# Kernel optimization log

Hardware: AMD Instinct MI355X
Metric: run time of the kernel (lower is better)

## Reference

```python
import jax, jax.numpy as jnp
import numpy as np

H_OUT = 512
W_OUT = 512


def _leaky(x):
    return jnp.where(x >= 0, x, 0.2 * x)


def _spline(cp, out_size):
    # cp: [B, R, N] control points -> [B, R, out_size] cubic Hermite interp
    N = cp.shape[-1]
    nseg = N - 1
    eps = 1e-3
    t = jnp.linspace(eps, 1.0 - eps, out_size)
    ts = t * nseg
    seg = jnp.clip(jnp.floor(ts).astype(jnp.int32), 0, nseg - 1)
    tau = jnp.clip(ts - seg.astype(ts.dtype), 0.0, 0.9999)
    t2 = tau * tau
    t3 = t2 * tau
    h00 = 2 * t3 - 3 * t2 + 1
    h10 = t3 - 2 * t2 + tau
    h01 = -2 * t3 + 3 * t2
    h11 = t3 - t2
    # central-difference tangents, scaled by 1/num_segments
    m = jnp.concatenate([
        (cp[..., 1:2] - cp[..., 0:1]) * 0.5,
        (cp[..., 2:] - cp[..., :-2]) * 0.5,
        (cp[..., -1:] - cp[..., -2:-1]) * 0.5,
    ], axis=-1) / nseg
    seg1 = jnp.clip(seg + 1, 0, N - 1)
    pk = cp[..., seg]
    pk1 = cp[..., seg1]
    mk = m[..., seg]
    mk1 = m[..., seg1]
    return h00 * pk + h10 * mk + h01 * pk1 + h11 * mk1


def _gen(feats, w1, b1, w2, b2):
    # batched per-rank 2-layer MLP: feats [B,R,D], w1 [R,D,Hd], w2 [R,Hd,C]
    hdn = _leaky(jnp.einsum('brd,rdh->brh', feats, w1) + b1[None])
    return jnp.einsum('brh,rhc->brc', hdn, w2) + b2[None]


def setup_inputs() -> dict:
    key = jax.random.key(0)
    ks = iter(jax.random.split(key, 40))
    def rn(shape, s=0.05):
        return jax.random.normal(next(ks), shape, jnp.float32) * s
    B, D, Hd = 64, 768, 256
    Rm, Ra, CX, CY = 16, 8, 24, 24
    Rt = Rm + Ra
    inp = {
        'h': jax.random.normal(next(ks), (B, D), jnp.float32),
        'rank_emb': rn((Rt, Hd), 0.1),
        'st_w1': rn((D, 2 * Hd)), 'st_b1': jnp.zeros((2 * Hd,), jnp.float32),
        'st_w2': rn((2 * Hd, Hd)), 'st_b2': jnp.zeros((Hd,), jnp.float32),
        'rm_w1': rn((Rt, 2 * Hd, Hd)), 'rm_b1': jnp.zeros((Rt, Hd), jnp.float32),
        'rm_w2': rn((Rt, Hd, Hd)), 'rm_b2': jnp.zeros((Rt, Hd), jnp.float32),
        'mx_w1': rn((Rm, Hd, Hd)), 'mx_b1': jnp.zeros((Rm, Hd), jnp.float32),
        'mx_w2': rn((Rm, Hd, CX)), 'mx_b2': jnp.zeros((Rm, CX), jnp.float32),
        'my_w1': rn((Rm, Hd, Hd)), 'my_b1': jnp.zeros((Rm, Hd), jnp.float32),
        'my_w2': rn((Rm, Hd, CY)), 'my_b2': jnp.zeros((Rm, CY), jnp.float32),
        'ax_w1': rn((Ra, Hd, Hd)), 'ax_b1': jnp.zeros((Ra, Hd), jnp.float32),
        'ax_w2': rn((Ra, Hd, CX)), 'ax_b2': jnp.zeros((Ra, CX), jnp.float32),
        'ay_w1': rn((Ra, Hd, Hd)), 'ay_b1': jnp.zeros((Ra, Hd), jnp.float32),
        'ay_w2': rn((Ra, Hd, CY)), 'ay_b2': jnp.zeros((Ra, CY), jnp.float32),
        'mult_w': jnp.ones((Rm,), jnp.float32) / Rm,
        'addx_w': jnp.ones((Ra,), jnp.float32) / Ra * 0.5,
        'addy_w': jnp.ones((Ra,), jnp.float32) / Ra * 0.5,
        'gbias': jnp.asarray(0.5, jnp.float32),
    }
    return inp


def reference(h, rank_emb, st_w1, st_b1, st_w2, st_b2,
              rm_w1, rm_b1, rm_w2, rm_b2,
              mx_w1, mx_b1, mx_w2, mx_b2,
              my_w1, my_b1, my_w2, my_b2,
              ax_w1, ax_b1, ax_w2, ax_b2,
              ay_w1, ay_b1, ay_w2, ay_b2,
              mult_w, addx_w, addy_w, gbias):
    B = h.shape[0]
    Rt = rank_emb.shape[0]
    Rm = mx_w1.shape[0]
    # shared conditioning
    shared = _leaky(h @ st_w1 + st_b1) @ st_w2 + st_b2  # [B, Hd]
    comb = jnp.concatenate([
        jnp.broadcast_to(shared[:, None, :], (B, Rt, shared.shape[-1])),
        jnp.broadcast_to(rank_emb[None], (B, Rt, rank_emb.shape[-1])),
    ], axis=-1)  # [B, Rt, 2*Hd]
    rf = _gen(comb, rm_w1, rm_b1, rm_w2, rm_b2)  # [B, Rt, Hd]
    fm, fa = rf[:, :Rm], rf[:, Rm:]
    Px_m = _gen(fm, mx_w1, mx_b1, mx_w2, mx_b2)  # [B, Rm, CX]
    Py_m = _gen(fm, my_w1, my_b1, my_w2, my_b2)
    Px_a = _gen(fa, ax_w1, ax_b1, ax_w2, ax_b2)
    Py_a = _gen(fa, ay_w1, ay_b1, ay_w2, ay_b2)
    u = _spline(Px_m, W_OUT)   # [B, Rm, W]
    v = _spline(Py_m, H_OUT)   # [B, Rm, H]
    a_x = _spline(Px_a, W_OUT)
    b_y = _spline(Py_a, H_OUT)
    depth_mult = jnp.einsum('brw,brh,r->bhw', u, v, jax.nn.softmax(mult_w))
    dx = jnp.einsum('brw,r->bw', a_x, jax.nn.softmax(addx_w))
    dy = jnp.einsum('brh,r->bh', b_y, jax.nn.softmax(addy_w))
    depth = depth_mult + dx[:, None, :] + dy[:, :, None] + gbias
    return depth[:, None]  # [B, 1, H, W]
```

## Files before the change

kernel.cpp:

```cpp
#include <hip/hip_runtime.h>


__device__ __forceinline__ float leaky(float v) { return v >= 0.f ? v : 0.2f * v; }

__global__ __launch_bounds__(256, 2) void l1_kernel(
    const float* __restrict__ h, const float* __restrict__ W,
    const float* __restrict__ bias, float* __restrict__ outp)
{
    __shared__ __align__(16) float a_lds[128][34];
    __shared__ __align__(16) float w_lds[128][34];
    const int tid = threadIdx.x;
    const int x = blockIdx.x, z = blockIdx.z;
    const int b0 = (x & 1) * 32, n0 = (x >> 1) * 32;
    const int nq = tid & 15, bq = tid >> 4;
    const int k0 = z * 128;
    float a00, a01, a10, a11;
    if (z == 0) {
        float bv0 = bias[n0 + nq * 2], bv1 = bias[n0 + nq * 2 + 1];
        a00 = bv0; a01 = bv1; a10 = bv0; a11 = bv1;
    } else { a00 = a01 = a10 = a11 = 0.f; }
    #pragma unroll
    for (int j = 0; j < 16; ++j) {
        int idx = tid + j * 256;
        int k = idx & 127, c = idx >> 7;
        a_lds[k][c] = h[(size_t)(b0 + c) * 768 + k0 + k];
        int n = idx & 31, kk = idx >> 5;
        w_lds[kk][n] = W[(size_t)(k0 + kk) * 512 + n0 + n];
    }
    __syncthreads();
    #pragma unroll 32
    for (int kk = 0; kk < 128; ++kk) {
        float2 a = *(const float2*)&a_lds[kk][bq * 2];
        float2 w = *(const float2*)&w_lds[kk][nq * 2];
        a00 += a.x * w.x; a01 += a.x * w.y;
        a10 += a.y * w.x; a11 += a.y * w.y;
    }
    float* ob = outp + (size_t)z * 32768;
    ob[(size_t)(b0 + bq * 2) * 512 + n0 + nq * 2]         = a00;
    ob[(size_t)(b0 + bq * 2) * 512 + n0 + nq * 2 + 1]     = a01;
    ob[(size_t)(b0 + bq * 2 + 1) * 512 + n0 + nq * 2]     = a10;
    ob[(size_t)(b0 + bq * 2 + 1) * 512 + n0 + nq * 2 + 1] = a11;
}

__global__ __launch_bounds__(512, 1) void mega_kernel(
    const float* __restrict__ hid1p,
    const float* __restrict__ st_w2, const float* __restrict__ st_b2,
    const float* __restrict__ rank_emb,
    const float* __restrict__ rm_w1, const float* __restrict__ rm_b1,
    const float* __restrict__ rm_w2, const float* __restrict__ rm_b2,
    const float* __restrict__ mx_w1, const float* __restrict__ mx_b1,
    const float* __restrict__ mx_w2, const float* __restrict__ mx_b2,
    const float* __restrict__ my_w1, const float* __restrict__ my_b1,
    const float* __restrict__ my_w2, const float* __restrict__ my_b2,
    const float* __restrict__ ax_w1, const float* __restrict__ ax_b1,
    const float* __restrict__ ax_w2, const float* __restrict__ ax_b2,
    const float* __restrict__ ay_w1, const float* __restrict__ ay_b1,
    const float* __restrict__ ay_w2, const float* __restrict__ ay_b2,
    float* __restrict__ Pcat)
{
    __shared__ __align__(16) float hid_s[8][512];
    __shared__ __align__(16) float sh_s[8][256];
    __shared__ __align__(16) float hdn_s[8][256];
    __shared__ __align__(16) float rf_s[8][256];
    __shared__ __align__(16) float hc_s[2][8][256];
    __shared__ float re_s[256];
    __shared__ float remb_s[256];
    const int tid = threadIdx.x;
    const int blk = blockIdx.x;
    const int r = blk % 24;
    const int bt = blk / 24;
    const int b0 = bt * 8;
    const int col = tid & 255, rh = tid >> 8;
    const int r0 = rh * 4;

    {
        const float4* hp = (const float4*)hid1p;
        #pragma unroll
        for (int i = 0; i < 2; ++i) {
            int idx = tid + i * 512;
            int row = idx >> 7, j4 = idx & 127;
            size_t off = (size_t)(b0 + row) * 128 + j4;
            float4 v0 = hp[off],            v1 = hp[8192 + off],  v2 = hp[16384 + off];
            float4 v3 = hp[24576 + off],    v4 = hp[32768 + off], v5 = hp[40960 + off];
            float4 s;
            s.x = leaky(v0.x + v1.x + v2.x + v3.x + v4.x + v5.x);
            s.y = leaky(v0.y + v1.y + v2.y + v3.y + v4.y + v5.y);
            s.z = leaky(v0.z + v1.z + v2.z + v3.z + v4.z + v5.z);
            s.w = leaky(v0.w + v1.w + v2.w + v3.w + v4.w + v5.w);
            ((float4*)&hid_s[row][0])[j4] = s;
        }
    }
    if (tid < 256) remb_s[tid] = rank_emb[r * 256 + tid];
    __syncthreads();

    {
        float bv = st_b2[col];
        float a0 = bv, a1 = bv, a2 = bv, a3 = bv;
        const float* wp = st_w2 + col;
        #pragma unroll 4
        for (int d = 0; d < 512; d += 4) {
            float w0 = wp[(size_t)(d + 0) * 256], w1 = wp[(size_t)(d + 1) * 256];
            float w2 = wp[(size_t)(d + 2) * 256], w3 = wp[(size_t)(d + 3) * 256];
            float4 s0 = *(const float4*)&hid_s[r0 + 0][d];
            float4 s1 = *(const float4*)&hid_s[r0 + 1][d];
            float4 s2 = *(const float4*)&hid_s[r0 + 2][d];
            float4 s3 = *(const float4*)&hid_s[r0 + 3][d];
            a0 += s0.x * w0 + s0.y * w1 + s0.z * w2 + s0.w * w3;
            a1 += s1.x * w0 + s1.y * w1 + s1.z * w2 + s1.w * w3;
            a2 += s2.x * w0 + s2.y * w1 + s2.z * w2 + s2.w * w3;
            a3 += s3.x * w0 + s3.y * w1 + s3.z * w2 + s3.w * w3;
        }
        sh_s[r0 + 0][col] = a0; sh_s[r0 + 1][col] = a1;
        sh_s[r0 + 2][col] = a2; sh_s[r0 + 3][col] = a3;
    }
    __syncthreads();

    if (tid < 256) {
        float rb = rm_b1[r * 256 + col];
        const float* wb = rm_w1 + ((size_t)r * 512 + 256) * 256 + col;
        #pragma unroll 4
        for (int d = 0; d < 256; d += 4) {
            float w0 = wb[(size_t)(d + 0) * 256], w1 = wb[(size_t)(d + 1) * 256];
            float w2 = wb[(size_t)(d + 2) * 256], w3 = wb[(size_t)(d + 3) * 256];
            float4 e = *(const float4*)&remb_s[d];
            rb += e.x * w0 + e.y * w1 + e.z * w2 + e.w * w3;
        }
        re_s[col] = rb;
    }
    __syncthreads();

    {
        float bv = re_s[col];
        float a0 = bv, a1 = bv, a2 = bv, a3 = bv;
        const float* wp = rm_w1 + (size_t)r * 512 * 256 + col;
        #pragma unroll 4
        for (int d = 0; d < 256; d += 4) {
            float w0 = wp[(size_t)(d + 0) * 256], w1 = wp[(size_t)(d + 1) * 256];
            float w2 = wp[(size_t)(d + 2) * 256], w3 = wp[(size_t)(d + 3) * 256];
            float4 s0 = *(const float4*)&sh_s[r0 + 0][d];
            float4 s1 = *(const float4*)&sh_s[r0 + 1][d];
            float4 s2 = *(const float4*)&sh_s[r0 + 2][d];
            float4 s3 = *(const float4*)&sh_s[r0 + 3][d];
            a0 += s0.x * w0 + s0.y * w1 + s0.z * w2 + s0.w * w3;
            a1 += s1.x * w0 + s1.y * w1 + s1.z * w2 + s1.w * w3;
            a2 += s2.x * w0 + s2.y * w1 + s2.z * w2 + s2.w * w3;
            a3 += s3.x * w0 + s3.y * w1 + s3.z * w2 + s3.w * w3;
        }
        hdn_s[r0 + 0][col] = leaky(a0); hdn_s[r0 + 1][col] = leaky(a1);
        hdn_s[r0 + 2][col] = leaky(a2); hdn_s[r0 + 3][col] = leaky(a3);
    }
    __syncthreads();

    {
        float bv = rm_b2[r * 256 + col];
        float a0 = bv, a1 = bv, a2 = bv, a3 = bv;
        const float* wp = rm_w2 + (size_t)r * 65536 + col;
        #pragma unroll 4
        for (int d = 0; d < 256; d += 4) {
            float w0 = wp[(size_t)(d + 0) * 256], w1 = wp[(size_t)(d + 1) * 256];
            float w2 = wp[(size_t)(d + 2) * 256], w3 = wp[(size_t)(d + 3) * 256];
            float4 s0 = *(const float4*)&hdn_s[r0 + 0][d];
            float4 s1 = *(const float4*)&hdn_s[r0 + 1][d];
            float4 s2 = *(const float4*)&hdn_s[r0 + 2][d];
            float4 s3 = *(const float4*)&hdn_s[r0 + 3][d];
            a0 += s0.x * w0 + s0.y * w1 + s0.z * w2 + s0.w * w3;
            a1 += s1.x * w0 + s1.y * w1 + s1.z * w2 + s1.w * w3;
            a2 += s2.x * w0 + s2.y * w1 + s2.z * w2 + s2.w * w3;
            a3 += s3.x * w0 + s3.y * w1 + s3.z * w2 + s3.w * w3;
        }
        rf_s[r0 + 0][col] = a0; rf_s[r0 + 1][col] = a1;
        rf_s[r0 + 2][col] = a2; rf_s[r0 + 3][col] = a3;
    }
    __syncthreads();

    const float *W1, *B1, *W2, *B2; int y;
    if (r < 16) {
        if (rh == 0) { y = r;      W1 = mx_w1 + (size_t)r * 65536;  B1 = mx_b1 + r * 256;  W2 = mx_w2 + (size_t)r * 6144;  B2 = mx_b2 + r * 24; }
        else         { y = 16 + r; W1 = my_w1 + (size_t)r * 65536;  B1 = my_b1 + r * 256;  W2 = my_w2 + (size_t)r * 6144;  B2 = my_b2 + r * 24; }
    } else {
        int rw = r - 16;
        if (rh == 0) { y = 32 + rw; W1 = ax_w1 + (size_t)rw * 65536; B1 = ax_b1 + rw * 256; W2 = ax_w2 + (size_t)rw * 6144; B2 = ax_b2 + rw * 24; }
        else         { y = 40 + rw; W1 = ay_w1 + (size_t)rw * 65536; B1 = ay_b1 + rw * 256; W2 = ay_w2 + (size_t)rw * 6144; B2 = ay_b2 + rw * 24; }
    }

    {
        float bv = B1[col];
        float acc[8];
        #pragma unroll
        for (int i = 0; i < 8; ++i) acc[i] = bv;
        const float* wp = W1 + col;
        #pragma unroll 2
        for (int d = 0; d < 256; d += 4) {
            float w0 = wp[(size_t)(d + 0) * 256], w1 = wp[(size_t)(d + 1) * 256];
            float w2 = wp[(size_t)(d + 2) * 256], w3 = wp[(size_t)(d + 3) * 256];
            #pragma unroll
            for (int i = 0; i < 8; ++i) {
                float4 s = *(const float4*)&rf_s[i][d];
                acc[i] += s.x * w0 + s.y * w1 + s.z * w2 + s.w * w3;
            }
        }
        #pragma unroll
        for (int i = 0; i < 8; ++i) hc_s[rh][i][col] = leaky(acc[i]);
    }
    __syncthreads();

    if (col < 192) {
        int row = col / 24, cj = col - row * 24;
        float acc = B2[cj];
        const float* wp = W2 + cj;
        #pragma unroll 4
        for (int d = 0; d < 256; d += 4) {
            float w0 = wp[(size_t)(d + 0) * 24], w1 = wp[(size_t)(d + 1) * 24];
            float w2 = wp[(size_t)(d + 2) * 24], w3 = wp[(size_t)(d + 3) * 24];
            float4 s = *(const float4*)&hc_s[rh][row][d];
            acc += s.x * w0 + s.y * w1 + s.z * w2 + s.w * w3;
        }
        Pcat[(size_t)(b0 + row) * 1152 + y * 24 + cj] = acc;
    }
}

__global__ __launch_bounds__(256, 2) void depth_fused_kernel(
    const float* __restrict__ Pcat,
    const float* __restrict__ mult_w, const float* __restrict__ addx_w,
    const float* __restrict__ addy_w, const float* __restrict__ gbias,
    float* __restrict__ out)
{
    __shared__ float cp[48][25];
    __shared__ float sw[33];
    __shared__ __align__(16) float u_s[16][132];
    __shared__ __align__(16) float v_s[16][132];
    __shared__ float dx_s[128], dy_s[128];
    const int tid = threadIdx.x;
    const int b = blockIdx.z, h0 = blockIdx.y * 128, w0 = blockIdx.x * 128;
    for (int idx = tid; idx < 1152; idx += 256)
        cp[idx / 24][idx % 24] = Pcat[(size_t)b * 1152 + idx];
    if (tid == 0) {
        float e[16], m, s;
        m = -1e30f; for (int i = 0; i < 16; ++i) m = fmaxf(m, mult_w[i]);
        s = 0.f;    for (int i = 0; i < 16; ++i) { e[i] = __expf(mult_w[i] - m); s += e[i]; }
        for (int i = 0; i < 16; ++i) sw[i] = e[i] / s;
        m = -1e30f; for (int i = 0; i < 8; ++i) m = fmaxf(m, addx_w[i]);
        s = 0.f;    for (int i = 0; i < 8; ++i) { e[i] = __expf(addx_w[i] - m); s += e[i]; }
        for (int i = 0; i < 8; ++i) sw[16 + i] = e[i] / s;
        m = -1e30f; for (int i = 0; i < 8; ++i) m = fmaxf(m, addy_w[i]);
        s = 0.f;    for (int i = 0; i < 8; ++i) { e[i] = __expf(addy_w[i] - m); s += e[i]; }
        for (int i = 0; i < 8; ++i) sw[24 + i] = e[i] / s;
        sw[32] = gbias[0];
    }
    __syncthreads();
    {
        const int local = tid & 127;
        const int gpos = (tid < 128 ? w0 : h0) + local;
        const float eps = 0.001f;
        float t = eps + (float)gpos * ((1.f - 2.f * eps) / 511.f);
        float ts = t * 23.f;
        int seg = (int)ts; if (seg > 22) seg = 22;
        float tau = ts - (float)seg;
        tau = fminf(fmaxf(tau, 0.f), 0.9999f);
        float t2 = tau * tau, t3 = t2 * tau;
        float h00 = 2.f * t3 - 3.f * t2 + 1.f;
        float h10 = t3 - 2.f * t2 + tau;
        float h01 = -2.f * t3 + 3.f * t2;
        float h11 = t3 - t2;
        int sm1 = seg > 0 ? seg - 1 : 0;
        int s1 = seg + 1;
        int sp2 = s1 < 23 ? s1 + 1 : 23;
        const float msc = 0.5f / 23.f;
        auto spl = [&](int row) -> float {
            float pk = cp[row][seg], pk1 = cp[row][s1];
            float mk  = msc * (pk1 - cp[row][sm1]);
            float mk1 = msc * (cp[row][sp2] - pk);
            return h00 * pk + h10 * mk + h01 * pk1 + h11 * mk1;
        };
        if (tid < 128) {
            #pragma unroll
            for (int r = 0; r < 16; ++r) u_s[r][local] = sw[r] * spl(r);
            float dx = sw[32];
            #pragma unroll
            for (int r = 0; r < 8; ++r) dx += sw[16 + r] * spl(32 + r);
            dx_s[local] = dx;
        } else {
            #pragma unroll
            for (int r = 0; r < 16; ++r) v_s[r][local] = spl(16 + r);
            float dy = 0.f;
            #pragma unroll
            for (int r = 0; r < 8; ++r) dy += sw[24 + r] * spl(40 + r);
            dy_s[local] = dy;
        }
    }
    __syncthreads();
    const int tw = tid & 15, th = tid >> 4;
    float acc[8][8];
    #pragma unroll
    for (int i = 0; i < 8; ++i)
        #pragma unroll
        for (int j = 0; j < 8; ++j) acc[i][j] = 0.f;
    #pragma unroll
    for (int r = 0; r < 16; ++r) {
        float4 va0 = *(const float4*)&v_s[r][th * 8];
        float4 va1 = *(const float4*)&v_s[r][th * 8 + 4];
        float4 ub0 = *(const float4*)&u_s[r][tw * 8];
        float4 ub1 = *(const float4*)&u_s[r][tw * 8 + 4];
        float va[8] = {va0.x, va0.y, va0.z, va0.w, va1.x, va1.y, va1.z, va1.w};
        float ub[8] = {ub0.x, ub0.y, ub0.z, ub0.w, ub1.x, ub1.y, ub1.z, ub1.w};
        #pragma unroll
        for (int i = 0; i < 8; ++i)
            #pragma unroll
            for (int j = 0; j < 8; ++j)
                acc[i][j] += va[i] * ub[j];
    }
    #pragma unroll
    for (int i = 0; i < 8; ++i) {
        float dyh = dy_s[th * 8 + i];
        float* op = out + (size_t)b * 262144 + (size_t)(h0 + th * 8 + i) * 512 + w0 + tw * 8;
        float4 o0, o1;
        o0.x = acc[i][0] + dx_s[tw * 8 + 0] + dyh;
        o0.y = acc[i][1] + dx_s[tw * 8 + 1] + dyh;
        o0.z = acc[i][2] + dx_s[tw * 8 + 2] + dyh;
        o0.w = acc[i][3] + dx_s[tw * 8 + 3] + dyh;
        o1.x = acc[i][4] + dx_s[tw * 8 + 4] + dyh;
        o1.y = acc[i][5] + dx_s[tw * 8 + 5] + dyh;
        o1.z = acc[i][6] + dx_s[tw * 8 + 6] + dyh;
        o1.w = acc[i][7] + dx_s[tw * 8 + 7] + dyh;
        *(float4*)op = o0;
        *(float4*)(op + 4) = o1;
    }
}

extern "C" void kernel_launch(void* const* d_in, const int* in_sizes, int n_in,
                              void* d_out, int out_size, void* d_ws, size_t ws_size,
                              hipStream_t stream) {
    const float* in_h     = (const float*)d_in[0];
    const float* rank_emb = (const float*)d_in[1];
    const float* st_w1    = (const float*)d_in[2];
    const float* st_b1    = (const float*)d_in[3];
    const float* st_w2    = (const float*)d_in[4];
    const float* st_b2    = (const float*)d_in[5];
    const float* rm_w1    = (const float*)d_in[6];
    const float* rm_b1    = (const float*)d_in[7];
    const float* rm_w2    = (const float*)d_in[8];
    const float* rm_b2    = (const float*)d_in[9];
    const float* mx_w1    = (const float*)d_in[10];
    const float* mx_b1    = (const float*)d_in[11];
    const float* mx_w2    = (const float*)d_in[12];
    const float* mx_b2    = (const float*)d_in[13];
    const float* my_w1    = (const float*)d_in[14];
    const float* my_b1    = (const float*)d_in[15];
    const float* my_w2    = (const float*)d_in[16];
    const float* my_b2    = (const float*)d_in[17];
    const float* ax_w1    = (const float*)d_in[18];
    const float* ax_b1    = (const float*)d_in[19];
    const float* ax_w2    = (const float*)d_in[20];
    const float* ax_b2    = (const float*)d_in[21];
    const float* ay_w1    = (const float*)d_in[22];
    const float* ay_b1    = (const float*)d_in[23];
    const float* ay_w2    = (const float*)d_in[24];
    const float* ay_b2    = (const float*)d_in[25];
    const float* mult_w   = (const float*)d_in[26];
    const float* addx_w   = (const float*)d_in[27];
    const float* addy_w   = (const float*)d_in[28];
    const float* gbias    = (const float*)d_in[29];
    (void)in_sizes; (void)n_in; (void)out_size; (void)ws_size;

    float* ws = (float*)d_ws;
    float* hid1p = ws;
    float* Pcat  = ws + 196608;

    l1_kernel<<<dim3(32, 1, 6), 256, 0, stream>>>(in_h, st_w1, st_b1, hid1p);

    mega_kernel<<<192, 512, 0, stream>>>(
        hid1p, st_w2, st_b2, rank_emb,
        rm_w1, rm_b1, rm_w2, rm_b2,
        mx_w1, mx_b1, mx_w2, mx_b2,
        my_w1, my_b1, my_w2, my_b2,
        ax_w1, ax_b1, ax_w2, ax_b2,
        ay_w1, ay_b1, ay_w2, ay_b2,
        Pcat);

    depth_fused_kernel<<<dim3(4, 4, 64), 256, 0, stream>>>(
        Pcat, mult_w, addx_w, addy_w, gbias, (float*)d_out);
}
```

Measured before the change: 234.7 us.

## Split shared layer into own kernel and split-K mega kernel over 1024 threads

Moves the shared st_w2 layer out of the per-rank mega kernel into a separate l2_kernel, so it is computed once per batch row instead of being recomputed in every one of the 24 rank blocks. The mega kernel now runs 1024 threads and splits each matmul's K dimension across four thread groups, reducing the partial sums through shared memory. This gives more memory-level parallelism for the weight streaming. The cost is an extra kernel launch, more shared memory and more barriers per block.

```diff
diff --git a/kernel.cpp b/kernel.cpp
--- a/kernel.cpp
+++ b/kernel.cpp
@@ -42,9 +42,59 @@
     ob[(size_t)(b0 + bq * 2 + 1) * 512 + n0 + nq * 2 + 1] = a11;
 }
 
-__global__ __launch_bounds__(512, 1) void mega_kernel(
-    const float* __restrict__ hid1p,
-    const float* __restrict__ st_w2, const float* __restrict__ st_b2,
+__global__ __launch_bounds__(1024, 4) void l2_kernel(
+    const float* __restrict__ hid1p, const float* __restrict__ st_w2,
+    const float* __restrict__ st_b2, float* __restrict__ sh)
+{
+    __shared__ __align__(16) float hid_s[4][512];
+    __shared__ __align__(16) float ps2[4][4][256];
+    const int tid = threadIdx.x;
+    const int b0 = blockIdx.x * 4;
+    if (tid < 512) {
+        int row = tid >> 7, j4 = tid & 127;
+        const float4* hp = (const float4*)hid1p;
+        size_t off = (size_t)(b0 + row) * 128 + j4;
+        float4 v0 = hp[off],         v1 = hp[8192 + off],  v2 = hp[16384 + off];
+        float4 v3 = hp[24576 + off], v4 = hp[32768 + off], v5 = hp[40960 + off];
+        float4 s;
+        s.x = leaky(v0.x + v1.x + v2.x + v3.x + v4.x + v5.x);
+        s.y = leaky(v0.y + v1.y + v2.y + v3.y + v4.y + v5.y);
+        s.z = leaky(v0.z + v1.z + v2.z + v3.z + v4.z + v5.z);
+        s.w = leaky(v0.w + v1.w + v2.w + v3.w + v4.w + v5.w);
+        ((float4*)&hid_s[row][0])[j4] = s;
+    }
+    __syncthreads();
+    {
+        const int col = tid & 255, kg = tid >> 8;
+        float a0 = 0.f, a1 = 0.f, a2 = 0.f, a3 = 0.f;
+        const float* wp = st_w2 + (size_t)(kg * 128) * 256 + col;
+        const int o = kg * 128;
+        #pragma unroll 4
+        for (int d = 0; d < 128; d += 4) {
+            float w0 = wp[(size_t)(d + 0) * 256], w1 = wp[(size_t)(d + 1) * 256];
+            float w2 = wp[(size_t)(d + 2) * 256], w3 = wp[(size_t)(d + 3) * 256];
+            float4 s0 = *(const float4*)&hid_s[0][o + d];
+            float4 s1 = *(const float4*)&hid_s[1][o + d];
+            float4 s2 = *(const float4*)&hid_s[2][o + d];
+            float4 s3 = *(const float4*)&hid_s[3][o + d];
+            a0 += s0.x * w0 + s0.y * w1 + s0.z * w2 + s0.w * w3;
+            a1 += s1.x * w0 + s1.y * w1 + s1.z * w2 + s1.w * w3;
+            a2 += s2.x * w0 + s2.y * w1 + s2.z * w2 + s2.w * w3;
+            a3 += s3.x * w0 + s3.y * w1 + s3.z * w2 + s3.w * w3;
+        }
+        ps2[kg][0][col] = a0; ps2[kg][1][col] = a1;
+        ps2[kg][2][col] = a2; ps2[kg][3][col] = a3;
+    }
+    __syncthreads();
+    {
+        int row = tid >> 8, c = tid & 255;
+        sh[(size_t)(b0 + row) * 256 + c] = st_b2[c]
+            + ps2[0][row][c] + ps2[1][row][c] + ps2[2][row][c] + ps2[3][row][c];
+    }
+}
+
+__global__ __launch_bounds__(1024, 4) void mega_kernel(
+    const float* __restrict__ sh,
     const float* __restrict__ rank_emb,
     const float* __restrict__ rm_w1, const float* __restrict__ rm_b1,
     const float* __restrict__ rm_w2, const float* __restrict__ rm_b2,
@@ -58,164 +108,179 @@
     const float* __restrict__ ay_w2, const float* __restrict__ ay_b2,
     float* __restrict__ Pcat)
 {
-    __shared__ __align__(16) float hid_s[8][512];
     __shared__ __align__(16) float sh_s[8][256];
     __shared__ __align__(16) float hdn_s[8][256];
     __shared__ __align__(16) float rf_s[8][256];
     __shared__ __align__(16) float hc_s[2][8][256];
-    __shared__ float re_s[256];
-    __shared__ float remb_s[256];
+    __shared__ __align__(16) float ps[4][8][256];
+    __shared__ __align__(16) float pre_ps[4][256];
+    __shared__ __align__(16) float remb_s[256];
     const int tid = threadIdx.x;
     const int blk = blockIdx.x;
     const int r = blk % 24;
     const int bt = blk / 24;
     const int b0 = bt * 8;
-    const int col = tid & 255, rh = tid >> 8;
-    const int r0 = rh * 4;
-
-    {
-        const float4* hp = (const float4*)hid1p;
-        #pragma unroll
-        for (int i = 0; i < 2; ++i) {
-            int idx = tid + i * 512;
-            int row = idx >> 7, j4 = idx & 127;
-            size_t off = (size_t)(b0 + row) * 128 + j4;
-            float4 v0 = hp[off],            v1 = hp[8192 + off],  v2 = hp[16384 + off];
-            float4 v3 = hp[24576 + off],    v4 = hp[32768 + off], v5 = hp[40960 + off];
-            float4 s;
-            s.x = leaky(v0.x + v1.x + v2.x + v3.x + v4.x + v5.x);
-            s.y = leaky(v0.y + v1.y + v2.y + v3.y + v4.y + v5.y);
-            s.z = leaky(v0.z + v1.z + v2.z + v3.z + v4.z + v5.z);
-            s.w = leaky(v0.w + v1.w + v2.w + v3.w + v4.w + v5.w);
-            ((float4*)&hid_s[row][0])[j4] = s;
-        }
-    }
-    if (tid < 256) remb_s[tid] = rank_emb[r * 256 + tid];
-    __syncthreads();
-
-    {
-        float bv = st_b2[col];
-        float a0 = bv, a1 = bv, a2 = bv, a3 = bv;
-        const float* wp = st_w2 + col;
+    const int col = tid & 255;
+    const int sub = tid >> 8;
+
+    if (tid < 512) {
+        int row = tid >> 6, j4 = tid & 63;
+        ((float4*)&sh_s[row][0])[j4] = ((const float4*)sh)[(size_t)(b0 + row) * 64 + j4];
+    } else if (tid < 576) {
+        int j4 = tid - 512;
+        ((float4*)remb_s)[j4] = ((const float4*)rank_emb)[(size_t)r * 64 + j4];
+    }
+    __syncthreads();
+
+    {
+        float accp = 0.f;
+        const float* wb = rm_w1 + ((size_t)r * 512 + 256 + sub * 64) * 256 + col;
+        #pragma unroll 8
+        for (int d = 0; d < 64; d += 4) {
+            float w0 = wb[(size_t)(d + 0) * 256], w1 = wb[(size_t)(d + 1) * 256];
+            float w2 = wb[(size_t)(d + 2) * 256], w3 = wb[(size_t)(d + 3) * 256];
+            float4 e = *(const float4*)&remb_s[sub * 64 + d];
+            accp += e.x * w0 + e.y * w1 + e.z * w2 + e.w * w3;
+        }
+        pre_ps[sub][col] = accp;
+
+        float acc[8];
+        #pragma unroll
+        for (int i = 0; i < 8; ++i) acc[i] = 0.f;
+        const float* wp = rm_w1 + ((size_t)r * 512 + sub * 64) * 256 + col;
+        const int o = sub * 64;
         #pragma unroll 4
-        for (int d = 0; d < 512; d += 4) {
+        for (int d = 0; d < 64; d += 4) {
             float w0 = wp[(size_t)(d + 0) * 256], w1 = wp[(size_t)(d + 1) * 256];
             float w2 = wp[(size_t)(d + 2) * 256], w3 = wp[(size_t)(d + 3) * 256];
-            float4 s0 = *(const float4*)&hid_s[r0 + 0][d];
-            float4 s1 = *(const float4*)&hid_s[r0 + 1][d];
-            float4 s2 = *(const float4*)&hid_s[r0 + 2][d];
-            float4 s3 = *(const float4*)&hid_s[r0 + 3][d];
-            a0 += s0.x * w0 + s0.y * w1 + s0.z * w2 + s0.w * w3;
-            a1 += s1.x * w0 + s1.y * w1 + s1.z * w2 + s1.w * w3;
-            a2 += s2.x * w0 + s2.y * w1 + s2.z * w2 + s2.w * w3;
-            a3 += s3.x * w0 + s3.y * w1 + s3.z * w2 + s3.w * w3;
-        }
-        sh_s[r0 + 0][col] = a0; sh_s[r0 + 1][col] = a1;
-        sh_s[r0 + 2][col] = a2; sh_s[r0 + 3][col] = a3;
-    }
-    __syncthreads();
-
-    if (tid < 256) {
-        float rb = rm_b1[r * 256 + col];
-        const float* wb = rm_w1 + ((size_t)r * 512 + 256) * 256 + col;
+            #pragma unroll
+            for (int i = 0; i < 8; ++i) {
+                float4 s = *(const float4*)&sh_s[i][o + d];
+                acc[i] += s.x * w0 + s.y * w1 + s.z * w2 + s.w * w3;
+            }
+        }
+        #pragma unroll
+        for (int i = 0; i < 8; ++i) ps[sub][i][col] = acc[i];
+    }
+    __syncthreads();
+
+    #pragma unroll
+    for (int t = 0; t < 2; ++t) {
+        int o = tid + t * 1024;
+        int i = o >> 8, c = o & 255;
+        float v = rm_b1[r * 256 + c]
+                + pre_ps[0][c] + pre_ps[1][c] + pre_ps[2][c] + pre_ps[3][c]
+                + ps[0][i][c] + ps[1][i][c] + ps[2][i][c] + ps[3][i][c];
+        hdn_s[i][c] = leaky(v);
+    }
+    __syncthreads();
+
+    {
+        float acc[8];
+        #pragma unroll
+        for (int i = 0; i < 8; ++i) acc[i] = 0.f;
+        const float* wp = rm_w2 + (size_t)r * 65536 + (size_t)(sub * 64) * 256 + col;
+        const int o = sub * 64;
         #pragma unroll 4
-        for (int d = 0; d < 256; d += 4) {
-            float w0 = wb[(size_t)(d + 0) * 256], w1 = wb[(size_t)(d + 1) * 256];
-            float w2 = wb[(size_t)(d + 2) * 256], w3 = wb[(size_t)(d + 3) * 256];
-            float4 e = *(const float4*)&remb_s[d];
-            rb += e.x * w0 + e.y * w1 + e.z * w2 + e.w * w3;
-        }
-        re_s[col] = rb;
-    }
-    __syncthreads();
-
-    {
-        float bv = re_s[col];
-        float a0 = bv, a1 = bv, a2 = bv, a3 = bv;
-        const float* wp = rm_w1 + (size_t)r * 512 * 256 + col;
-        #pragma unroll 4
-        for (int d = 0; d < 256; d += 4) {
+        for (int d = 0; d < 64; d += 4) {
             float w0 = wp[(size_t)(d + 0) * 256], w1 = wp[(size_t)(d + 1) * 256];
             float w2 = wp[(size_t)(d + 2) * 256], w3 = wp[(size_t)(d + 3) * 256];
-            float4 s0 = *(const float4*)&sh_s[r0 + 0][d];
-            float4 s1 = *(const float4*)&sh_s[r0 + 1][d];
-            float4 s2 = *(const float4*)&sh_s[r0 + 2][d];
-            float4 s3 = *(const float4*)&sh_s[r0 + 3][d];
-            a0 += s0.x * w0 + s0.y * w1 + s0.z * w2 + s0.w * w3;
-            a1 += s1.x * w0 + s1.y * w1 + s1.z * w2 + s1.w * w3;
-            a2 += s2.x * w0 + s2.y * w1 + s2.z * w2 + s2.w * w3;
-            a3 += s3.x * w0 + s3.y * w1 + s3.z * w2 + s3.w * w3;
-        }
-        hdn_s[r0 + 0][col] = leaky(a0); hdn_s[r0 + 1][col] = leaky(a1);
-        hdn_s[r0 + 2][col] = leaky(a2); hdn_s[r0 + 3][col] = leaky(a3);
-    }
-    __syncthreads();
-
-    {
-        float bv = rm_b2[r * 256 + col];
-        float a0 = bv, a1 = bv, a2 = bv, a3 = bv;
-        const float* wp = rm_w2 + (size_t)r * 65536 + col;
+            #pragma unroll
+            for (int i = 0; i < 8; ++i) {
+                float4 s = *(const float4*)&hdn_s[i][o + d];
+                acc[i] += s.x * w0 + s.y * w1 + s.z * w2 + s.w * w3;
+            }
+        }
+        #pragma unroll
+        for (int i = 0; i < 8; ++i) ps[sub][i][col] = acc[i];
+    }
+    __syncthreads();
+
+    #pragma unroll
+    for (int t = 0; t < 2; ++t) {
+        int o = tid + t * 1024;
+        int i = o >> 8, c = o & 255;
+        rf_s[i][c] = rm_b2[r * 256 + c]
+                   + ps[0][i][c] + ps[1][i][c] + ps[2][i][c] + ps[3][i][c];
+    }
+    __syncthreads();
+
+    const float *W1_0, *B1_0, *W2_0, *B2_0, *W1_1, *B1_1, *W2_1, *B2_1;
+    int y0, y1;
+    if (r < 16) {
+        y0 = r;       W1_0 = mx_w1 + (size_t)r * 65536;  B1_0 = mx_b1 + r * 256;
+                      W2_0 = mx_w2 + (size_t)r * 6144;   B2_0 = mx_b2 + r * 24;
+        y1 = 16 + r;  W1_1 = my_w1 + (size_t)r * 65536;  B1_1 = my_b1 + r * 256;
+                      W2_1 = my_w2 + (size_t)r * 6144;   B2_1 = my_b2 + r * 24;
+    } else {
+        int rw = r - 16;
+        y0 = 32 + rw; W1_0 = ax_w1 + (size_t)rw * 65536; B1_0 = ax_b1 + rw * 256;
+                      W2_0 = ax_w2 + (size_t)rw * 6144;  B2_0 = ax_b2 + rw * 24;
+        y1 = 40 + rw; W1_1 = ay_w1 + (size_t)rw * 65536; B1_1 = ay_b1 + rw * 256;
+                      W2_1 = ay_w2 + (size_t)rw * 6144;  B2_1 = ay_b2 + rw * 24;
+    }
+
+    {
+        const int h = sub & 1, kg = sub >> 1;
+        const float* wp = (h ? W1_1 : W1_0) + (size_t)(kg * 128) * 256 + col;
+        const int o = kg * 128;
+        float acc[8];
+        #pragma unroll
+        for (int i = 0; i < 8; ++i) acc[i] = 0.f;
         #pragma unroll 4
-        for (int d = 0; d < 256; d += 4) {
+        for (int d = 0; d < 128; d += 4) {
             float w0 = wp[(size_t)(d + 0) * 256], w1 = wp[(size_t)(d + 1) * 256];
             float w2 = wp[(size_t)(d + 2) * 256], w3 = wp[(size_t)(d + 3) * 256];
-            float4 s0 = *(const float4*)&hdn_s[r0 + 0][d];
-            float4 s1 = *(const float4*)&hdn_s[r0 + 1][d];
-            float4 s2 = *(const float4*)&hdn_s[r0 + 2][d];
-            float4 s3 = *(const float4*)&hdn_s[r0 + 3][d];
-            a0 += s0.x * w0 + s0.y * w1 + s0.z * w2 + s0.w * w3;
-            a1 += s1.x * w0 + s1.y * w1 + s1.z * w2 + s1.w * w3;
-            a2 += s2.x * w0 + s2.y * w1 + s2.z * w2 + s2.w * w3;
-            a3 += s3.x * w0 + s3.y * w1 + s3.z * w2 + s3.w * w3;
-        }
-        rf_s[r0 + 0][col] = a0; rf_s[r0 + 1][col] = a1;
-        rf_s[r0 + 2][col] = a2; rf_s[r0 + 3][col] = a3;
-    }
-    __syncthreads();
-
-    const float *W1, *B1, *W2, *B2; int y;
-    if (r < 16) {
-        if (rh == 0) { y = r;      W1 = mx_w1 + (size_t)r * 65536;  B1 = mx_b1 + r * 256;  W2 = mx_w2 + (size_t)r * 6144;  B2 = mx_b2 + r * 24; }
-        else         { y = 16 + r; W1 = my_w1 + (size_t)r * 65536;  B1 = my_b1 + r * 256;  W2 = my_w2 + (size_t)r * 6144;  B2 = my_b2 + r * 24; }
-    } else {
-        int rw = r - 16;
-        if (rh == 0) { y = 32 + rw; W1 = ax_w1 + (size_t)rw * 65536; B1 = ax_b1 + rw * 256; W2 = ax_w2 + (size_t)rw * 6144; B2 = ax_b2 + rw * 24; }
-        else         { y = 40 + rw; W1 = ay_w1 + (size_t)rw * 65536; B1 = ay_b1 + rw * 256; W2 = ay_w2 + (size_t)rw * 6144; B2 = ay_b2 + rw * 24; }
-    }
-
-    {
-        float bv = B1[col];
-        float acc[8];
-        #pragma unroll
-        for (int i = 0; i < 8; ++i) acc[i] = bv;
-        const float* wp = W1 + col;
-        #pragma unroll 2
-        for (int d = 0; d < 256; d += 4) {
-            float w0 = wp[(size_t)(d + 0) * 256], w1 = wp[(size_t)(d + 1) * 256];
-            float w2 = wp[(size_t)(d + 2) * 256], w3 = wp[(size_t)(d + 3) * 256];
             #pragma unroll
             for (int i = 0; i < 8; ++i) {
-                float4 s = *(const float4*)&rf_s[i][d];
+                float4 s = *(const float4*)&rf_s[i][o + d];
                 acc[i] += s.x * w0 + s.y * w1 + s.z * w2 + s.w * w3;
             }
         }
         #pragma unroll
-        for (int i = 0; i < 8; ++i) hc_s[rh][i][col] = leaky(acc[i]);
-    }
-    __syncthreads();
-
-    if (col < 192) {
-        int row = col / 24, cj = col - row * 24;
-        float acc = B2[cj];
-        const float* wp = W2 + cj;
-        #pragma unroll 4
-        for (int d = 0; d < 256; d += 4) {
-            float w0 = wp[(size_t)(d + 0) * 24], w1 = wp[(size_t)(d + 1) * 24];
-            float w2 = wp[(size_t)(d + 2) * 24], w3 = wp[(size_t)(d + 3) * 24];
-            float4 s = *(const float4*)&hc_s[rh][row][d];
+        for (int i = 0; i < 8; ++i) ps[sub][i][col] = acc[i];
+    }
+    __syncthreads();
+
+    {
+        const int h = sub & 1, i0 = (sub >> 1) * 4;
+        float bv = (h ? B1_1 : B1_0)[col];
+        #pragma unroll
+        for (int q = 0; q < 4; ++q) {
+            int i = i0 + q;
+            hc_s[h][i][col] = leaky(bv + ps[h][i][col] + ps[2 + h][i][col]);
+        }
+    }
+    __syncthreads();
+
+    float* psf = &ps[0][0][0];
+    if (tid < 768) {
+        int h = tid >= 384 ? 1 : 0;
+        int q = tid - h * 384;
+        int kg = q & 1;
+        int c2 = q >> 1;
+        int row = c2 / 24, cj = c2 - row * 24;
+        const float* wp = (h ? W2_1 : W2_0) + (size_t)(kg * 128) * 24 + cj;
+        const float* hp = &hc_s[h][row][kg * 128];
+        float acc = 0.f;
+        #pragma unroll 8
+        for (int d = 0; d < 128; d += 4) {
+            float w0 = wp[(d + 0) * 24], w1 = wp[(d + 1) * 24];
+            float w2 = wp[(d + 2) * 24], w3 = wp[(d + 3) * 24];
+            float4 s = *(const float4*)&hp[d];
             acc += s.x * w0 + s.y * w1 + s.z * w2 + s.w * w3;
         }
-        Pcat[(size_t)(b0 + row) * 1152 + y * 24 + cj] = acc;
+        psf[tid] = acc;
+    }
+    __syncthreads();
+
+    if (tid < 384) {
+        int h = tid >= 192 ? 1 : 0;
+        int c2 = tid - h * 192;
+        int row = c2 / 24, cj = c2 - row * 24;
+        float v = (h ? B2_1 : B2_0)[cj] + psf[h * 384 + c2 * 2] + psf[h * 384 + c2 * 2 + 1];
+        int y = h ? y1 : y0;
+        Pcat[(size_t)(b0 + row) * 1152 + y * 24 + cj] = v;
     }
 }
 
@@ -365,11 +430,14 @@
     float* ws = (float*)d_ws;
     float* hid1p = ws;
     float* Pcat  = ws + 196608;
+    float* shbuf = ws + 270336;
 
     l1_kernel<<<dim3(32, 1, 6), 256, 0, stream>>>(in_h, st_w1, st_b1, hid1p);
 
-    mega_kernel<<<192, 512, 0, stream>>>(
-        hid1p, st_w2, st_b2, rank_emb,
+    l2_kernel<<<16, 1024, 0, stream>>>(hid1p, st_w2, st_b2, shbuf);
+
+    mega_kernel<<<192, 1024, 0, stream>>>(
+        shbuf, rank_emb,
         rm_w1, rm_b1, rm_w2, rm_b2,
         mx_w1, mx_b1, mx_w2, mx_b2,
         my_w1, my_b1, my_w2, my_b2,
```

Result: slower. 298.3 us (+27.1%).

## Split shared-trunk layer into separate kernel and halve batch tile in mega kernel

Applied to the files above, without the earlier changes.

Moves the second shared MLP layer (st_w2) out of the per-rank mega kernel into its own small kernel that writes the shared features to workspace. Before this, each of the 24 rank blocks recomputed that layer for its batch tile. The mega kernel now handles 4 batch rows per block instead of 8, doubling the grid to 384 blocks, and uses less LDS so more blocks fit per CU. It also splits the rank-embedding projection across both thread halves. The cost is an extra kernel launch and each weight row being reloaded by twice as many blocks.

```diff
diff --git a/kernel.cpp b/kernel.cpp
--- a/kernel.cpp
+++ b/kernel.cpp
@@ -42,9 +42,53 @@
     ob[(size_t)(b0 + bq * 2 + 1) * 512 + n0 + nq * 2 + 1] = a11;
 }
 
-__global__ __launch_bounds__(512, 1) void mega_kernel(
-    const float* __restrict__ hid1p,
-    const float* __restrict__ st_w2, const float* __restrict__ st_b2,
+__global__ __launch_bounds__(512, 2) void l2_kernel(
+    const float* __restrict__ hid1p, const float* __restrict__ st_w2,
+    const float* __restrict__ st_b2, float* __restrict__ sh)
+{
+    __shared__ __align__(16) float hid_s[2][512];
+    __shared__ __align__(16) float ps2[2][2][256];
+    const int tid = threadIdx.x;
+    const int b0 = blockIdx.x * 2;
+    if (tid < 256) {
+        int row = tid >> 7, j4 = tid & 127;
+        const float4* hp = (const float4*)hid1p;
+        size_t off = (size_t)(b0 + row) * 128 + j4;
+        float4 v0 = hp[off],         v1 = hp[8192 + off],  v2 = hp[16384 + off];
+        float4 v3 = hp[24576 + off], v4 = hp[32768 + off], v5 = hp[40960 + off];
+        float4 s;
+        s.x = leaky(v0.x + v1.x + v2.x + v3.x + v4.x + v5.x);
+        s.y = leaky(v0.y + v1.y + v2.y + v3.y + v4.y + v5.y);
+        s.z = leaky(v0.z + v1.z + v2.z + v3.z + v4.z + v5.z);
+        s.w = leaky(v0.w + v1.w + v2.w + v3.w + v4.w + v5.w);
+        ((float4*)&hid_s[row][0])[j4] = s;
+    }
+    __syncthreads();
+    {
+        const int col = tid & 255, kg = tid >> 8;
+        const int o = kg * 256;
+        float a0 = 0.f, a1 = 0.f;
+        const float* wp = st_w2 + (size_t)o * 256 + col;
+        #pragma unroll 4
+        for (int d = 0; d < 256; d += 4) {
+            float w0 = wp[(size_t)(d + 0) * 256], w1 = wp[(size_t)(d + 1) * 256];
+            float w2 = wp[(size_t)(d + 2) * 256], w3 = wp[(size_t)(d + 3) * 256];
+            float4 s0 = *(const float4*)&hid_s[0][o + d];
+            float4 s1 = *(const float4*)&hid_s[1][o + d];
+            a0 += s0.x * w0 + s0.y * w1 + s0.z * w2 + s0.w * w3;
+            a1 += s1.x * w0 + s1.y * w1 + s1.z * w2 + s1.w * w3;
+        }
+        ps2[kg][0][col] = a0; ps2[kg][1][col] = a1;
+    }
+    __syncthreads();
+    {
+        int row = tid >> 8, c = tid & 255;
+        sh[(size_t)(b0 + row) * 256 + c] = st_b2[c] + ps2[0][row][c] + ps2[1][row][c];
+    }
+}
+
+__global__ __launch_bounds__(512, 4) void mega_kernel(
+    const float* __restrict__ sh,
     const float* __restrict__ rank_emb,
     const float* __restrict__ rm_w1, const float* __restrict__ rm_b1,
     const float* __restrict__ rm_w2, const float* __restrict__ rm_b2,
@@ -58,80 +102,46 @@
     const float* __restrict__ ay_w2, const float* __restrict__ ay_b2,
     float* __restrict__ Pcat)
 {
-    __shared__ __align__(16) float hid_s[8][512];
-    __shared__ __align__(16) float sh_s[8][256];
-    __shared__ __align__(16) float hdn_s[8][256];
-    __shared__ __align__(16) float rf_s[8][256];
-    __shared__ __align__(16) float hc_s[2][8][256];
-    __shared__ float re_s[256];
-    __shared__ float remb_s[256];
+    __shared__ __align__(16) float sh_s[4][256];
+    __shared__ __align__(16) float hdn_s[4][256];
+    __shared__ __align__(16) float rf_s[4][256];
+    __shared__ __align__(16) float hc_s[2][4][256];
+    __shared__ __align__(16) float re_ps[2][256];
+    __shared__ __align__(16) float remb_s[256];
     const int tid = threadIdx.x;
     const int blk = blockIdx.x;
     const int r = blk % 24;
     const int bt = blk / 24;
-    const int b0 = bt * 8;
+    const int b0 = bt * 4;
     const int col = tid & 255, rh = tid >> 8;
-    const int r0 = rh * 4;
-
-    {
-        const float4* hp = (const float4*)hid1p;
-        #pragma unroll
-        for (int i = 0; i < 2; ++i) {
-            int idx = tid + i * 512;
-            int row = idx >> 7, j4 = idx & 127;
-            size_t off = (size_t)(b0 + row) * 128 + j4;
-            float4 v0 = hp[off],            v1 = hp[8192 + off],  v2 = hp[16384 + off];
-            float4 v3 = hp[24576 + off],    v4 = hp[32768 + off], v5 = hp[40960 + off];
-            float4 s;
-            s.x = leaky(v0.x + v1.x + v2.x + v3.x + v4.x + v5.x);
-            s.y = leaky(v0.y + v1.y + v2.y + v3.y + v4.y + v5.y);
-            s.z = leaky(v0.z + v1.z + v2.z + v3.z + v4.z + v5.z);
-            s.w = leaky(v0.w + v1.w + v2.w + v3.w + v4.w + v5.w);
-            ((float4*)&hid_s[row][0])[j4] = s;
-        }
-    }
-    if (tid < 256) remb_s[tid] = rank_emb[r * 256 + tid];
-    __syncthreads();
-
-    {
-        float bv = st_b2[col];
-        float a0 = bv, a1 = bv, a2 = bv, a3 = bv;
-        const float* wp = st_w2 + col;
-        #pragma unroll 4
-        for (int d = 0; d < 512; d += 4) {
-            float w0 = wp[(size_t)(d + 0) * 256], w1 = wp[(size_t)(d + 1) * 256];
-            float w2 = wp[(size_t)(d + 2) * 256], w3 = wp[(size_t)(d + 3) * 256];
-            float4 s0 = *(const float4*)&hid_s[r0 + 0][d];
-            float4 s1 = *(const float4*)&hid_s[r0 + 1][d];
-            float4 s2 = *(const float4*)&hid_s[r0 + 2][d];
-            float4 s3 = *(const float4*)&hid_s[r0 + 3][d];
-            a0 += s0.x * w0 + s0.y * w1 + s0.z * w2 + s0.w * w3;
-            a1 += s1.x * w0 + s1.y * w1 + s1.z * w2 + s1.w * w3;
-            a2 += s2.x * w0 + s2.y * w1 + s2.z * w2 + s2.w * w3;
-            a3 += s3.x * w0 + s3.y * w1 + s3.z * w2 + s3.w * w3;
-        }
-        sh_s[r0 + 0][col] = a0; sh_s[r0 + 1][col] = a1;
-        sh_s[r0 + 2][col] = a2; sh_s[r0 + 3][col] = a3;
-    }
-    __syncthreads();
+    const int r0 = rh * 2;
 
     if (tid < 256) {
-        float rb = rm_b1[r * 256 + col];
-        const float* wb = rm_w1 + ((size_t)r * 512 + 256) * 256 + col;
-        #pragma unroll 4
-        for (int d = 0; d < 256; d += 4) {
+        ((float4*)sh_s)[tid] = ((const float4*)sh)[(size_t)b0 * 64 + tid];
+    } else if (tid < 320) {
+        int j4 = tid - 256;
+        ((float4*)remb_s)[j4] = ((const float4*)rank_emb)[(size_t)r * 64 + j4];
+    }
+    __syncthreads();
+
+    {
+        float accp = 0.f;
+        const float* wb = rm_w1 + ((size_t)r * 512 + 256 + rh * 128) * 256 + col;
+        const int o = rh * 128;
+        #pragma unroll 4
+        for (int d = 0; d < 128; d += 4) {
             float w0 = wb[(size_t)(d + 0) * 256], w1 = wb[(size_t)(d + 1) * 256];
             float w2 = wb[(size_t)(d + 2) * 256], w3 = wb[(size_t)(d + 3) * 256];
-            float4 e = *(const float4*)&remb_s[d];
-            rb += e.x * w0 + e.y * w1 + e.z * w2 + e.w * w3;
-        }
-        re_s[col] = rb;
-    }
-    __syncthreads();
-
-    {
-        float bv = re_s[col];
-        float a0 = bv, a1 = bv, a2 = bv, a3 = bv;
+            float4 e = *(const float4*)&remb_s[o + d];
+            accp += e.x * w0 + e.y * w1 + e.z * w2 + e.w * w3;
+        }
+        re_ps[rh][col] = accp;
+    }
+    __syncthreads();
+
+    {
+        float bv = rm_b1[r * 256 + col] + re_ps[0][col] + re_ps[1][col];
+        float a0 = bv, a1 = bv;
         const float* wp = rm_w1 + (size_t)r * 512 * 256 + col;
         #pragma unroll 4
         for (int d = 0; d < 256; d += 4) {
@@ -139,21 +149,16 @@
             float w2 = wp[(size_t)(d + 2) * 256], w3 = wp[(size_t)(d + 3) * 256];
             float4 s0 = *(const float4*)&sh_s[r0 + 0][d];
             float4 s1 = *(const float4*)&sh_s[r0 + 1][d];
-            float4 s2 = *(const float4*)&sh_s[r0 + 2][d];
-            float4 s3 = *(const float4*)&sh_s[r0 + 3][d];
             a0 += s0.x * w0 + s0.y * w1 + s0.z * w2 + s0.w * w3;
             a1 += s1.x * w0 + s1.y * w1 + s1.z * w2 + s1.w * w3;
-            a2 += s2.x * w0 + s2.y * w1 + s2.z * w2 + s2.w * w3;
-            a3 += s3.x * w0 + s3.y * w1 + s3.z * w2 + s3.w * w3;
         }
         hdn_s[r0 + 0][col] = leaky(a0); hdn_s[r0 + 1][col] = leaky(a1);
-        hdn_s[r0 + 2][col] = leaky(a2); hdn_s[r0 + 3][col] = leaky(a3);
     }
     __syncthreads();
 
     {
         float bv = rm_b2[r * 256 + col];
-        float a0 = bv, a1 = bv, a2 = bv, a3 = bv;
+        float a0 = bv, a1 = bv;
         const float* wp = rm_w2 + (size_t)r * 65536 + col;
         #pragma unroll 4
         for (int d = 0; d < 256; d += 4) {
@@ -161,15 +166,10 @@
             float w2 = wp[(size_t)(d + 2) * 256], w3 = wp[(size_t)(d + 3) * 256];
             float4 s0 = *(const float4*)&hdn_s[r0 + 0][d];
             float4 s1 = *(const float4*)&hdn_s[r0 + 1][d];
-            float4 s2 = *(const float4*)&hdn_s[r0 + 2][d];
-            float4 s3 = *(const float4*)&hdn_s[r0 + 3][d];
             a0 += s0.x * w0 + s0.y * w1 + s0.z * w2 + s0.w * w3;
             a1 += s1.x * w0 + s1.y * w1 + s1.z * w2 + s1.w * w3;
-            a2 += s2.x * w0 + s2.y * w1 + s2.z * w2 + s2.w * w3;
-            a3 += s3.x * w0 + s3.y * w1 + s3.z * w2 + s3.w * w3;
         }
         rf_s[r0 + 0][col] = a0; rf_s[r0 + 1][col] = a1;
-        rf_s[r0 + 2][col] = a2; rf_s[r0 + 3][col] = a3;
     }
     __syncthreads();
 
@@ -185,26 +185,26 @@
 
     {
         float bv = B1[col];
-        float acc[8];
+        float acc[4];
         #pragma unroll
-        for (int i = 0; i < 8; ++i) acc[i] = bv;
+        for (int i = 0; i < 4; ++i) acc[i] = bv;
         const float* wp = W1 + col;
-        #pragma unroll 2
+        #pragma unroll 4
         for (int d = 0; d < 256; d += 4) {
             float w0 = wp[(size_t)(d + 0) * 256], w1 = wp[(size_t)(d + 1) * 256];
             float w2 = wp[(size_t)(d + 2) * 256], w3 = wp[(size_t)(d + 3) * 256];
             #pragma unroll
-            for (int i = 0; i < 8; ++i) {
+            for (int i = 0; i < 4; ++i) {
                 float4 s = *(const float4*)&rf_s[i][d];
                 acc[i] += s.x * w0 + s.y * w1 + s.z * w2 + s.w * w3;
             }
         }
         #pragma unroll
-        for (int i = 0; i < 8; ++i) hc_s[rh][i][col] = leaky(acc[i]);
-    }
-    __syncthreads();
-
-    if (col < 192) {
+        for (int i = 0; i < 4; ++i) hc_s[rh][i][col] = leaky(acc[i]);
+    }
+    __syncthreads();
+
+    if (col < 96) {
         int row = col / 24, cj = col - row * 24;
         float acc = B2[cj];
         const float* wp = W2 + cj;
@@ -365,11 +365,14 @@
     float* ws = (float*)d_ws;
     float* hid1p = ws;
     float* Pcat  = ws + 196608;
+    float* shbuf = ws + 270336;
 
     l1_kernel<<<dim3(32, 1, 6), 256, 0, stream>>>(in_h, st_w1, st_b1, hid1p);
 
-    mega_kernel<<<192, 512, 0, stream>>>(
-        hid1p, st_w2, st_b2, rank_emb,
+    l2_kernel<<<32, 512, 0, stream>>>(hid1p, st_w2, st_b2, shbuf);
+
+    mega_kernel<<<384, 512, 0, stream>>>(
+        shbuf, rank_emb,
         rm_w1, rm_b1, rm_w2, rm_b2,
         mx_w1, mx_b1, mx_w2, mx_b2,
         my_w1, my_b1, my_w2, my_b2,
```

Result: slower. 240.1 us (+2.3%).
